# Optimization experiments

Hardware: AMD Instinct MI355X
Metric: run time of the kernel (lower is better)

The kernel has to match this reference:

```python
import jax, jax.numpy as jnp
import numpy as np

B, D, E, C = 16384, 2048, 16, 64  # batch, feat_dim, num_experts, classes per expert
CLASS_STARTS = np.arange(E, dtype=np.int32) * C  # contiguous equal-size class ranges


def setup_inputs() -> dict:
    key = jax.random.key(0)
    k1, k2, k3, k4, k5 = jax.random.split(key, 5)
    return {
        "features": jax.random.normal(k1, (B, D), dtype=jnp.float32),
        "coarse_w": jax.random.normal(k2, (E, D), dtype=jnp.float32) * 0.02,
        "coarse_b": jax.random.normal(k3, (E,), dtype=jnp.float32) * 0.02,
        "expert_w": jax.random.normal(k4, (E, C, D), dtype=jnp.float32) * 0.02,
        "expert_b": jax.random.normal(k5, (E, C), dtype=jnp.float32) * 0.02,
    }


def reference(features, coarse_w, coarse_b, expert_w, expert_b):
    # coarse router: Linear(feat_dim -> num_experts)
    coarse_output = features @ coarse_w.T + coarse_b          # [B, E]
    expert_id = jnp.argmax(coarse_output, axis=1)             # [B] top-1 routing

    # all-expert heads as one batched GEMM, then select routed expert per sample
    # (same math as gather-by-mask + per-expert Linear + scatter-back loop)
    y_all = jnp.einsum('bd,ecd->bec', features, expert_w) + expert_b  # [B, E, C]
    y = jnp.take_along_axis(y_all, expert_id[:, None, None], axis=1)[:, 0, :]  # [B, C]

    # local_preds: softmax probs of the routed expert (all experts have C = max classes)
    local_preds = jax.nn.softmax(y, axis=1)                   # [B, C]

    # global prediction = local argmax + expert's class-range start
    starts = jnp.asarray(CLASS_STARTS)
    global_preds = (jnp.argmax(y, axis=1) + starts[expert_id]).astype(jnp.float32)  # [B]

    return coarse_output, expert_id, local_preds, global_preds
```

## Files before the change

kernel.cpp:

```cpp
#include <hip/hip_runtime.h>
#include <cstdint>

static constexpr int B_ = 16384;
static constexpr int D_ = 2048;
static constexpr int E_ = 16;
static constexpr int C_ = 64;
static constexpr int KCH = 32;
static constexpr int TR_E = 64;
static constexpr int SK_E = 4;
static constexpr int TR_C = 128;
static constexpr int SK_C = 8;
static constexpr int MAXITEMS = (B_ / TR_E) + E_;

template <int RPT, int CPT, int NC, int TR, int SK, bool FLAT>
__global__ __launch_bounds__(256) void gemm_tile(
    const float* __restrict__ feat, const float* __restrict__ Wall,
    const int* __restrict__ rowList, const int* __restrict__ cnt,
    const int* __restrict__ sched, const int* __restrict__ nItems,
    float* __restrict__ part0,
    float* __restrict__ partRest)
{
  constexpr int FITER = TR / 32;
  constexpr int WSLOTS = NC * 8;
  constexpr int WITER = (WSLOTS + 255) / 256;
  constexpr int CG = NC / CPT;

  __shared__ float fT[KCH * TR];
  __shared__ float wT[KCH * NC];
  __shared__ int rIdx[TR];

  const int tid = threadIdx.x;
  int e, tile, kz;
  if (FLAT) {
    const int b = blockIdx.x;
    kz = b % SK;
    const int item = b / SK;
    if (item >= *nItems) return;
    const int s = sched[item];
    e = s & 255;
    tile = s >> 8;
  } else {
    e = 0;
    tile = blockIdx.x;
    kz = blockIdx.z;
  }
  const int count = cnt ? cnt[e] : B_;

  if (tid < TR) {
    const int slot = tile * TR + tid;
    rIdx[tid] = (slot < count) ? (rowList ? rowList[e * B_ + slot] : slot) : 0;
  }
  __syncthreads();

  unsigned grows[FITER];
  int dcf[FITER], sbf[FITER];
#pragma unroll
  for (int i = 0; i < FITER; ++i) {
    const int idx = i * 256 + tid;
    const int rl = idx >> 3;
    dcf[i] = idx & 7;
    grows[i] = (unsigned)rIdx[rl];
    sbf[i] = (((rl >> 3) ^ dcf[i]) << 3) + (rl & 7);
  }
  int wc[WITER], wdc[WITER], wsb[WITER];
  bool wact[WITER];
#pragma unroll
  for (int i = 0; i < WITER; ++i) {
    const int idx = i * 256 + tid;
    wact[i] = idx < WSLOTS;
    const int c = (idx < WSLOTS) ? (idx >> 3) : 0;
    wc[i] = c;
    wdc[i] = idx & 7;
    wsb[i] = (((c >> 3) ^ (wdc[i] & (NC / 8 - 1))) << 3) + (c & 7);
  }

  const int cg = tid % CG;
  const int rg = tid / CG;

  float acc[RPT][CPT];
#pragma unroll
  for (int r = 0; r < RPT; ++r)
#pragma unroll
    for (int c = 0; c < CPT; ++c) acc[r][c] = 0.f;

  const float* We = Wall + (size_t)e * NC * D_;
  constexpr int KRANGE = D_ / SK;
  constexpr int NCH = KRANGE / KCH;
  const int k0 = kz * KRANGE;

  float4 pf[FITER], pw[WITER];
#pragma unroll
  for (int i = 0; i < FITER; ++i)
    pf[i] = *(const float4*)(feat + (size_t)grows[i] * D_ + k0 + dcf[i] * 4);
#pragma unroll
  for (int i = 0; i < WITER; ++i)
    if (wact[i])
      pw[i] = *(const float4*)(We + (size_t)wc[i] * D_ + k0 + wdc[i] * 4);

  for (int ch = 0; ch < NCH; ++ch) {
#pragma unroll
    for (int i = 0; i < FITER; ++i) {
      float* p = &fT[(dcf[i] * 4) * TR + sbf[i]];
      p[0 * TR] = pf[i].x;
      p[1 * TR] = pf[i].y;
      p[2 * TR] = pf[i].z;
      p[3 * TR] = pf[i].w;
    }
#pragma unroll
    for (int i = 0; i < WITER; ++i)
      if (wact[i]) {
        float* p = &wT[(wdc[i] * 4) * NC + wsb[i]];
        p[0 * NC] = pw[i].x;
        p[1 * NC] = pw[i].y;
        p[2 * NC] = pw[i].z;
        p[3 * NC] = pw[i].w;
      }
    __syncthreads();
    if (ch + 1 < NCH) {
      const int kb = k0 + (ch + 1) * KCH;
#pragma unroll
      for (int i = 0; i < FITER; ++i)
        pf[i] = *(const float4*)(feat + (size_t)grows[i] * D_ + kb + dcf[i] * 4);
#pragma unroll
      for (int i = 0; i < WITER; ++i)
        if (wact[i])
          pw[i] = *(const float4*)(We + (size_t)wc[i] * D_ + kb + wdc[i] * 4);
    }
#pragma unroll
    for (int dd = 0; dd < KCH; ++dd) {
      const int s = dd >> 2;
      const int sw = s & (NC / 8 - 1);
      float a[RPT], bb[CPT];
#pragma unroll
      for (int r4 = 0; r4 < RPT / 4; ++r4) {
        const int col = rg * RPT + r4 * 4;
        const float4 v =
            *(const float4*)&fT[dd * TR + (((col >> 3) ^ s) << 3) + (col & 7)];
        a[r4 * 4 + 0] = v.x;
        a[r4 * 4 + 1] = v.y;
        a[r4 * 4 + 2] = v.z;
        a[r4 * 4 + 3] = v.w;
      }
      if constexpr (CPT >= 4) {
#pragma unroll
        for (int c4 = 0; c4 < CPT / 4; ++c4) {
          const int col = cg * CPT + c4 * 4;
          const float4 v =
              *(const float4*)&wT[dd * NC + (((col >> 3) ^ sw) << 3) + (col & 7)];
          bb[c4 * 4 + 0] = v.x;
          bb[c4 * 4 + 1] = v.y;
          bb[c4 * 4 + 2] = v.z;
          bb[c4 * 4 + 3] = v.w;
        }
      } else {
        const int col = cg * 2;
        const float2 v =
            *(const float2*)&wT[dd * NC + (((col >> 3) ^ sw) << 3) + (col & 7)];
        bb[0] = v.x;
        bb[1] = v.y;
      }
#pragma unroll
      for (int r = 0; r < RPT; ++r)
#pragma unroll
        for (int c = 0; c < CPT; ++c) acc[r][c] += a[r] * bb[c];
    }
    __syncthreads();
  }

  float* pk = kz ? (partRest + (size_t)(kz - 1) * B_ * NC) : part0;
#pragma unroll
  for (int r = 0; r < RPT; ++r) {
    const int lrow = rg * RPT + r;
    const int slot = tile * TR + lrow;
    if (slot < count) {
      const int grow = rIdx[lrow];
      float* dst = pk + (size_t)grow * NC + cg * CPT;
      if constexpr (CPT >= 4) {
#pragma unroll
        for (int c4 = 0; c4 < CPT / 4; ++c4)
          *(float4*)(dst + c4 * 4) =
              make_float4(acc[r][c4 * 4 + 0], acc[r][c4 * 4 + 1],
                          acc[r][c4 * 4 + 2], acc[r][c4 * 4 + 3]);
      } else {
        *(float2*)dst = make_float2(acc[r][0], acc[r][1]);
      }
    }
  }
}

__global__ __launch_bounds__(256) void coarse_finish(
    const float* __restrict__ cpart0, const float* __restrict__ cpartRest,
    const float* __restrict__ cb, float* __restrict__ out0,
    float* __restrict__ out1, int* __restrict__ eidArr, int* __restrict__ cnt,
    int* __restrict__ rowList) {
  __shared__ int lcnt[E_];
  __shared__ int lbase[E_];
  const int tid = threadIdx.x;
  if (tid < E_) lcnt[tid] = 0;
  __syncthreads();
  const int row = blockIdx.x * 256 + tid;

  float v[E_];
#pragma unroll
  for (int j = 0; j < E_; ++j) v[j] = cb[j];
#pragma unroll
  for (int kz = 0; kz < SK_C; ++kz) {
    const float* p = (kz == 0) ? (cpart0 + (size_t)row * E_)
                               : (cpartRest + ((size_t)(kz - 1) * B_ + row) * E_);
#pragma unroll
    for (int j4 = 0; j4 < E_ / 4; ++j4) {
      const float4 t = *(const float4*)(p + j4 * 4);
      v[j4 * 4 + 0] += t.x;
      v[j4 * 4 + 1] += t.y;
      v[j4 * 4 + 2] += t.z;
      v[j4 * 4 + 3] += t.w;
    }
  }
  int best = 0;
  float bv = v[0];
#pragma unroll
  for (int j = 1; j < E_; ++j)
    if (v[j] > bv) { bv = v[j]; best = j; }

  float* o0 = out0 + (size_t)row * E_;
#pragma unroll
  for (int j4 = 0; j4 < E_ / 4; ++j4)
    *(float4*)(o0 + j4 * 4) = make_float4(v[j4 * 4 + 0], v[j4 * 4 + 1],
                                          v[j4 * 4 + 2], v[j4 * 4 + 3]);
  out1[row] = (float)best;
  eidArr[row] = best;

  const int lpos = atomicAdd(&lcnt[best], 1);
  __syncthreads();
  if (tid < E_) lbase[tid] = atomicAdd(&cnt[tid], lcnt[tid]);
  __syncthreads();
  rowList[best * B_ + lbase[best] + lpos] = row;
}

__global__ void make_schedule(const int* __restrict__ cnt,
                              int* __restrict__ sched,
                              int* __restrict__ nItems) {
  __shared__ int tiles[E_];
  __shared__ int offs[E_];
  const int t = threadIdx.x;
  if (t < E_) tiles[t] = (cnt[t] + TR_E - 1) / TR_E;
  __syncthreads();
  if (t == 0) {
    int acc = 0;
    for (int e = 0; e < E_; ++e) {
      offs[e] = acc;
      acc += tiles[e];
    }
    *nItems = acc;
  }
  __syncthreads();
  if (t < E_) {
    const int o = offs[t], n = tiles[t];
    for (int k = 0; k < n; ++k) sched[o + k] = t | (k << 8);
  }
}

__global__ __launch_bounds__(256) void finish_rows(
    const float* __restrict__ ypart0, const float* __restrict__ ypartRest,
    const float* __restrict__ eb, const int* __restrict__ eidArr,
    float* __restrict__ out2, float* __restrict__ out3) {
  const int lane = threadIdx.x & 63;
  const int row = (blockIdx.x * 256 + threadIdx.x) >> 6;
  const int eid = eidArr[row];

  float v = eb[eid * C_ + lane];
  v += ypart0[(size_t)row * C_ + lane];
#pragma unroll
  for (int kz = 1; kz < SK_E; ++kz)
    v += ypartRest[((size_t)(kz - 1) * B_ + row) * C_ + lane];

  float m = v;
#pragma unroll
  for (int off = 32; off; off >>= 1) m = fmaxf(m, __shfl_xor(m, off, 64));
  const float p = __expf(v - m);
  float s = p;
#pragma unroll
  for (int off = 32; off; off >>= 1) s += __shfl_xor(s, off, 64);
  out2[(size_t)row * C_ + lane] = p / s;

  float av = v;
  int ai = lane;
#pragma unroll
  for (int off = 32; off; off >>= 1) {
    const float ov = __shfl_xor(av, off, 64);
    const int oi = __shfl_xor(ai, off, 64);
    if (ov > av || (ov == av && oi < ai)) { av = ov; ai = oi; }
  }
  if (lane == 0) out3[row] = (float)(ai + (eid << 6));
}

extern "C" void kernel_launch(void* const* d_in, const int* in_sizes, int n_in,
                              void* d_out, int out_size, void* d_ws,
                              size_t ws_size, hipStream_t stream) {
  const float* feat = (const float*)d_in[0];
  const float* cw = (const float*)d_in[1];
  const float* cb = (const float*)d_in[2];
  const float* ew = (const float*)d_in[3];
  const float* eb = (const float*)d_in[4];

  float* out0 = (float*)d_out;
  float* out1 = out0 + (size_t)B_ * E_;
  float* out2 = out1 + B_;
  float* out3 = out2 + (size_t)B_ * C_;

  char* ws = (char*)d_ws;
  float* cpartRest = (float*)ws;
  float* ypartRest = cpartRest + (size_t)(SK_C - 1) * B_ * E_;
  int* rowList = (int*)(ypartRest + (size_t)(SK_E - 1) * B_ * C_);
  int* cnt = rowList + (size_t)E_ * B_;
  int* eidArr = cnt + 64;
  int* sched = eidArr + B_;
  int* nItems = sched + 512;

  hipMemsetAsync(cnt, 0, E_ * sizeof(int), stream);

  gemm_tile<4, 2, E_, TR_C, SK_C, false>
      <<<dim3(B_ / TR_C, 1, SK_C), 256, 0, stream>>>(
          feat, cw, nullptr, nullptr, nullptr, nullptr, out0, cpartRest);
  coarse_finish<<<B_ / 256, 256, 0, stream>>>(out0, cpartRest, cb, out0, out1,
                                              eidArr, cnt, rowList);
  make_schedule<<<1, 64, 0, stream>>>(cnt, sched, nItems);
  gemm_tile<4, 4, C_, TR_E, SK_E, true>
      <<<MAXITEMS * SK_E, 256, 0, stream>>>(feat, ew, rowList, cnt, sched,
                                            nItems, out2, ypartRest);
  finish_rows<<<(B_ * 64) / 256, 256, 0, stream>>>(out2, ypartRest, eb, eidArr,
                                                   out2, out3);
}
```

Baseline: 298.9 us.

## Fuse coarse router GEMM, argmax, bucketing and scheduling into one kernel

Replaces the split-K coarse GEMM, coarse_finish and make_schedule kernels with a single coarse_fused kernel. In it, each wave computes 4 full rows with a register shuffle-transpose reduction, then does the argmax and row bucketing, and the last block (found via an atomic done counter) builds the expert schedule. This removes two launches and the partial-sum round trip through global memory. The expert GEMM is also changed to a K chunk of 64, which halves its sync/chunk count at the cost of more shared memory. The risks are lower parallelism in the coarse GEMM (1024 blocks, each re-reading the full coarse weights from cache) and the correctness burden of the last-block pattern.

```diff
diff --git a/kernel.cpp b/kernel.cpp
--- a/kernel.cpp
+++ b/kernel.cpp
@@ -5,50 +5,212 @@
 static constexpr int D_ = 2048;
 static constexpr int E_ = 16;
 static constexpr int C_ = 64;
-static constexpr int KCH = 32;
 static constexpr int TR_E = 64;
 static constexpr int SK_E = 4;
-static constexpr int TR_C = 128;
-static constexpr int SK_C = 8;
+static constexpr int KCH_E = 64;
 static constexpr int MAXITEMS = (B_ / TR_E) + E_;
 
-template <int RPT, int CPT, int NC, int TR, int SK, bool FLAT>
-__global__ __launch_bounds__(256) void gemm_tile(
+__global__ __launch_bounds__(256) void coarse_fused(
+    const float* __restrict__ feat, const float* __restrict__ cw,
+    const float* __restrict__ cb, float* __restrict__ out0,
+    float* __restrict__ out1, int* __restrict__ eidArr, int* __restrict__ cnt,
+    int* __restrict__ done, int* __restrict__ rowList,
+    int* __restrict__ sched, int* __restrict__ nItems) {
+  __shared__ int lcnt[E_];
+  __shared__ int lbase[E_];
+  __shared__ int rowE[16];
+  __shared__ int rowP[16];
+  __shared__ int lastFlag;
+
+  const int tid = threadIdx.x;
+  const int lane = tid & 63;
+  const int wv = tid >> 6;
+  if (tid < E_) lcnt[tid] = 0;
+  if (tid == 0) lastFlag = 0;
+  __syncthreads();
+
+  const int rowBase = blockIdx.x * 16 + wv * 4;
+  const int le = ((lane & 1) << 3) | ((lane & 2) << 1) | ((lane & 4) >> 1) |
+                 ((lane & 8) >> 3);
+  const float cbr = cb[le];
+
+  const float* rp[4];
+#pragma unroll
+  for (int r = 0; r < 4; ++r)
+    rp[r] = feat + (size_t)(rowBase + r) * D_ + lane * 4;
+
+  float acc[4][16];
+#pragma unroll
+  for (int r = 0; r < 4; ++r)
+#pragma unroll
+    for (int j = 0; j < 16; ++j) acc[r][j] = 0.f;
+
+  float4 pf[4];
+#pragma unroll
+  for (int r = 0; r < 4; ++r) pf[r] = *(const float4*)(rp[r]);
+
+  for (int c = 0; c < 8; ++c) {
+    float4 f[4];
+#pragma unroll
+    for (int r = 0; r < 4; ++r) f[r] = pf[r];
+    if (c < 7) {
+#pragma unroll
+      for (int r = 0; r < 4; ++r)
+        pf[r] = *(const float4*)(rp[r] + (c + 1) * 256);
+    }
+    const float* wb = cw + c * 256 + lane * 4;
+#pragma unroll
+    for (int e4 = 0; e4 < 4; ++e4) {
+      float4 w[4];
+#pragma unroll
+      for (int j = 0; j < 4; ++j)
+        w[j] = *(const float4*)(wb + (size_t)(e4 * 4 + j) * D_);
+#pragma unroll
+      for (int j = 0; j < 4; ++j)
+#pragma unroll
+        for (int r = 0; r < 4; ++r) {
+          acc[r][e4 * 4 + j] += f[r].x * w[j].x;
+          acc[r][e4 * 4 + j] += f[r].y * w[j].y;
+          acc[r][e4 * 4 + j] += f[r].z * w[j].z;
+          acc[r][e4 * 4 + j] += f[r].w * w[j].w;
+        }
+    }
+  }
+
+#pragma unroll
+  for (int r = 0; r < 4; ++r) {
+    float v[16];
+#pragma unroll
+    for (int j = 0; j < 16; ++j) v[j] = acc[r][j];
+    {
+      const bool hi = lane & 1;
+#pragma unroll
+      for (int j = 0; j < 8; ++j) {
+        const float a = v[j], b = v[j + 8];
+        v[j] = hi ? b : a;
+        v[j + 8] = hi ? a : b;
+      }
+#pragma unroll
+      for (int j = 0; j < 8; ++j) v[j] += __shfl_xor(v[j + 8], 1);
+    }
+    {
+      const bool hi = lane & 2;
+#pragma unroll
+      for (int j = 0; j < 4; ++j) {
+        const float a = v[j], b = v[j + 4];
+        v[j] = hi ? b : a;
+        v[j + 4] = hi ? a : b;
+      }
+#pragma unroll
+      for (int j = 0; j < 4; ++j) v[j] += __shfl_xor(v[j + 4], 2);
+    }
+    {
+      const bool hi = lane & 4;
+#pragma unroll
+      for (int j = 0; j < 2; ++j) {
+        const float a = v[j], b = v[j + 2];
+        v[j] = hi ? b : a;
+        v[j + 2] = hi ? a : b;
+      }
+#pragma unroll
+      for (int j = 0; j < 2; ++j) v[j] += __shfl_xor(v[j + 2], 4);
+    }
+    {
+      const bool hi = lane & 8;
+      const float a = v[0], b = v[1];
+      v[0] = hi ? b : a;
+      v[1] = hi ? a : b;
+      v[0] += __shfl_xor(v[1], 8);
+    }
+    v[0] += __shfl_xor(v[0], 16);
+    v[0] += __shfl_xor(v[0], 32);
+    const float val = v[0] + cbr;
+
+    const int row = rowBase + r;
+    if (lane < 16) out0[(size_t)row * E_ + le] = val;
+
+    float mv = val;
+    int mi = le;
+#pragma unroll
+    for (int d = 1; d <= 8; d <<= 1) {
+      const float ov = __shfl_xor(mv, d);
+      const int oi = __shfl_xor(mi, d);
+      if (ov > mv || (ov == mv && oi < mi)) {
+        mv = ov;
+        mi = oi;
+      }
+    }
+    if (lane == 0) {
+      out1[row] = (float)mi;
+      eidArr[row] = mi;
+      const int p = atomicAdd(&lcnt[mi], 1);
+      rowE[wv * 4 + r] = mi;
+      rowP[wv * 4 + r] = p;
+    }
+  }
+  __syncthreads();
+  if (tid < E_) lbase[tid] = atomicAdd(&cnt[tid], lcnt[tid]);
+  __syncthreads();
+  if (tid < 16) {
+    const int e = rowE[tid], p = rowP[tid];
+    rowList[e * B_ + lbase[e] + p] = blockIdx.x * 16 + tid;
+  }
+
+  __threadfence();
+  if (tid == 0) {
+    if (atomicAdd(done, 1) == (int)gridDim.x - 1) lastFlag = 1;
+  }
+  __syncthreads();
+  if (lastFlag) {
+    if (tid < E_) lcnt[tid] = (atomicAdd(&cnt[tid], 0) + TR_E - 1) / TR_E;
+    __syncthreads();
+    if (tid == 0) {
+      int a = 0;
+      for (int e = 0; e < E_; ++e) {
+        lbase[e] = a;
+        a += lcnt[e];
+      }
+      *nItems = a;
+    }
+    __syncthreads();
+    if (tid < E_) {
+      const int o = lbase[tid], n = lcnt[tid];
+      for (int k = 0; k < n; ++k) sched[o + k] = tid | (k << 8);
+    }
+  }
+}
+
+template <int RPT, int CPT, int NC, int TR, int SK, int KCH>
+__global__ __launch_bounds__(256) void gemm_expert(
     const float* __restrict__ feat, const float* __restrict__ Wall,
     const int* __restrict__ rowList, const int* __restrict__ cnt,
     const int* __restrict__ sched, const int* __restrict__ nItems,
-    float* __restrict__ part0,
-    float* __restrict__ partRest)
-{
-  constexpr int FITER = TR / 32;
-  constexpr int WSLOTS = NC * 8;
+    float* __restrict__ part0, float* __restrict__ partRest) {
+  constexpr int DCB = KCH / 4;
+  constexpr int FITER = TR * DCB / 256;
+  constexpr int WSLOTS = NC * DCB;
   constexpr int WITER = (WSLOTS + 255) / 256;
   constexpr int CG = NC / CPT;
+  constexpr int RB = TR / 8;
+  constexpr int CB = NC / 8;
 
   __shared__ float fT[KCH * TR];
   __shared__ float wT[KCH * NC];
   __shared__ int rIdx[TR];
 
   const int tid = threadIdx.x;
-  int e, tile, kz;
-  if (FLAT) {
-    const int b = blockIdx.x;
-    kz = b % SK;
-    const int item = b / SK;
-    if (item >= *nItems) return;
-    const int s = sched[item];
-    e = s & 255;
-    tile = s >> 8;
-  } else {
-    e = 0;
-    tile = blockIdx.x;
-    kz = blockIdx.z;
-  }
-  const int count = cnt ? cnt[e] : B_;
+  const int b = blockIdx.x;
+  const int kz = b % SK;
+  const int item = b / SK;
+  if (item >= *nItems) return;
+  const int s = sched[item];
+  const int e = s & 255;
+  const int tile = s >> 8;
+  const int count = cnt[e];
 
   if (tid < TR) {
     const int slot = tile * TR + tid;
-    rIdx[tid] = (slot < count) ? (rowList ? rowList[e * B_ + slot] : slot) : 0;
+    rIdx[tid] = (slot < count) ? rowList[e * B_ + slot] : 0;
   }
   __syncthreads();
 
@@ -57,21 +219,19 @@
 #pragma unroll
   for (int i = 0; i < FITER; ++i) {
     const int idx = i * 256 + tid;
-    const int rl = idx >> 3;
-    dcf[i] = idx & 7;
+    const int rl = idx / DCB;
+    dcf[i] = idx % DCB;
     grows[i] = (unsigned)rIdx[rl];
-    sbf[i] = (((rl >> 3) ^ dcf[i]) << 3) + (rl & 7);
+    sbf[i] = (((rl >> 3) ^ (dcf[i] & (RB - 1))) << 3) + (rl & 7);
   }
   int wc[WITER], wdc[WITER], wsb[WITER];
-  bool wact[WITER];
 #pragma unroll
   for (int i = 0; i < WITER; ++i) {
     const int idx = i * 256 + tid;
-    wact[i] = idx < WSLOTS;
-    const int c = (idx < WSLOTS) ? (idx >> 3) : 0;
+    const int c = idx / DCB;
     wc[i] = c;
-    wdc[i] = idx & 7;
-    wsb[i] = (((c >> 3) ^ (wdc[i] & (NC / 8 - 1))) << 3) + (c & 7);
+    wdc[i] = idx % DCB;
+    wsb[i] = (((c >> 3) ^ (wdc[i] & (CB - 1))) << 3) + (c & 7);
   }
 
   const int cg = tid % CG;
@@ -94,8 +254,7 @@
     pf[i] = *(const float4*)(feat + (size_t)grows[i] * D_ + k0 + dcf[i] * 4);
 #pragma unroll
   for (int i = 0; i < WITER; ++i)
-    if (wact[i])
-      pw[i] = *(const float4*)(We + (size_t)wc[i] * D_ + k0 + wdc[i] * 4);
+    pw[i] = *(const float4*)(We + (size_t)wc[i] * D_ + k0 + wdc[i] * 4);
 
   for (int ch = 0; ch < NCH; ++ch) {
 #pragma unroll
@@ -107,14 +266,13 @@
       p[3 * TR] = pf[i].w;
     }
 #pragma unroll
-    for (int i = 0; i < WITER; ++i)
-      if (wact[i]) {
-        float* p = &wT[(wdc[i] * 4) * NC + wsb[i]];
-        p[0 * NC] = pw[i].x;
-        p[1 * NC] = pw[i].y;
-        p[2 * NC] = pw[i].z;
-        p[3 * NC] = pw[i].w;
-      }
+    for (int i = 0; i < WITER; ++i) {
+      float* p = &wT[(wdc[i] * 4) * NC + wsb[i]];
+      p[0 * NC] = pw[i].x;
+      p[1 * NC] = pw[i].y;
+      p[2 * NC] = pw[i].z;
+      p[3 * NC] = pw[i].w;
+    }
     __syncthreads();
     if (ch + 1 < NCH) {
       const int kb = k0 + (ch + 1) * KCH;
@@ -123,41 +281,32 @@
         pf[i] = *(const float4*)(feat + (size_t)grows[i] * D_ + kb + dcf[i] * 4);
 #pragma unroll
       for (int i = 0; i < WITER; ++i)
-        if (wact[i])
-          pw[i] = *(const float4*)(We + (size_t)wc[i] * D_ + kb + wdc[i] * 4);
+        pw[i] = *(const float4*)(We + (size_t)wc[i] * D_ + kb + wdc[i] * 4);
     }
 #pragma unroll
     for (int dd = 0; dd < KCH; ++dd) {
-      const int s = dd >> 2;
-      const int sw = s & (NC / 8 - 1);
+      const int sz = (dd >> 2) & (RB - 1);
+      const int sw = (dd >> 2) & (CB - 1);
       float a[RPT], bb[CPT];
 #pragma unroll
       for (int r4 = 0; r4 < RPT / 4; ++r4) {
         const int col = rg * RPT + r4 * 4;
         const float4 v =
-            *(const float4*)&fT[dd * TR + (((col >> 3) ^ s) << 3) + (col & 7)];
+            *(const float4*)&fT[dd * TR + (((col >> 3) ^ sz) << 3) + (col & 7)];
         a[r4 * 4 + 0] = v.x;
         a[r4 * 4 + 1] = v.y;
         a[r4 * 4 + 2] = v.z;
         a[r4 * 4 + 3] = v.w;
       }
-      if constexpr (CPT >= 4) {
-#pragma unroll
-        for (int c4 = 0; c4 < CPT / 4; ++c4) {
-          const int col = cg * CPT + c4 * 4;
-          const float4 v =
-              *(const float4*)&wT[dd * NC + (((col >> 3) ^ sw) << 3) + (col & 7)];
-          bb[c4 * 4 + 0] = v.x;
-          bb[c4 * 4 + 1] = v.y;
-          bb[c4 * 4 + 2] = v.z;
-          bb[c4 * 4 + 3] = v.w;
-        }
-      } else {
-        const int col = cg * 2;
-        const float2 v =
-            *(const float2*)&wT[dd * NC + (((col >> 3) ^ sw) << 3) + (col & 7)];
-        bb[0] = v.x;
-        bb[1] = v.y;
+#pragma unroll
+      for (int c4 = 0; c4 < CPT / 4; ++c4) {
+        const int col = cg * CPT + c4 * 4;
+        const float4 v =
+            *(const float4*)&wT[dd * NC + (((col >> 3) ^ sw) << 3) + (col & 7)];
+        bb[c4 * 4 + 0] = v.x;
+        bb[c4 * 4 + 1] = v.y;
+        bb[c4 * 4 + 2] = v.z;
+        bb[c4 * 4 + 3] = v.w;
       }
 #pragma unroll
       for (int r = 0; r < RPT; ++r)
@@ -175,88 +324,12 @@
     if (slot < count) {
       const int grow = rIdx[lrow];
       float* dst = pk + (size_t)grow * NC + cg * CPT;
-      if constexpr (CPT >= 4) {
-#pragma unroll
-        for (int c4 = 0; c4 < CPT / 4; ++c4)
-          *(float4*)(dst + c4 * 4) =
-              make_float4(acc[r][c4 * 4 + 0], acc[r][c4 * 4 + 1],
-                          acc[r][c4 * 4 + 2], acc[r][c4 * 4 + 3]);
-      } else {
-        *(float2*)dst = make_float2(acc[r][0], acc[r][1]);
-      }
-    }
-  }
-}
-
-__global__ __launch_bounds__(256) void coarse_finish(
-    const float* __restrict__ cpart0, const float* __restrict__ cpartRest,
-    const float* __restrict__ cb, float* __restrict__ out0,
-    float* __restrict__ out1, int* __restrict__ eidArr, int* __restrict__ cnt,
-    int* __restrict__ rowList) {
-  __shared__ int lcnt[E_];
-  __shared__ int lbase[E_];
-  const int tid = threadIdx.x;
-  if (tid < E_) lcnt[tid] = 0;
-  __syncthreads();
-  const int row = blockIdx.x * 256 + tid;
-
-  float v[E_];
-#pragma unroll
-  for (int j = 0; j < E_; ++j) v[j] = cb[j];
-#pragma unroll
-  for (int kz = 0; kz < SK_C; ++kz) {
-    const float* p = (kz == 0) ? (cpart0 + (size_t)row * E_)
-                               : (cpartRest + ((size_t)(kz - 1) * B_ + row) * E_);
-#pragma unroll
-    for (int j4 = 0; j4 < E_ / 4; ++j4) {
-      const float4 t = *(const float4*)(p + j4 * 4);
-      v[j4 * 4 + 0] += t.x;
-      v[j4 * 4 + 1] += t.y;
-      v[j4 * 4 + 2] += t.z;
-      v[j4 * 4 + 3] += t.w;
-    }
-  }
-  int best = 0;
-  float bv = v[0];
-#pragma unroll
-  for (int j = 1; j < E_; ++j)
-    if (v[j] > bv) { bv = v[j]; best = j; }
-
-  float* o0 = out0 + (size_t)row * E_;
-#pragma unroll
-  for (int j4 = 0; j4 < E_ / 4; ++j4)
-    *(float4*)(o0 + j4 * 4) = make_float4(v[j4 * 4 + 0], v[j4 * 4 + 1],
-                                          v[j4 * 4 + 2], v[j4 * 4 + 3]);
-  out1[row] = (float)best;
-  eidArr[row] = best;
-
-  const int lpos = atomicAdd(&lcnt[best], 1);
-  __syncthreads();
-  if (tid < E_) lbase[tid] = atomicAdd(&cnt[tid], lcnt[tid]);
-  __syncthreads();
-  rowList[best * B_ + lbase[best] + lpos] = row;
-}
-
-__global__ void make_schedule(const int* __restrict__ cnt,
-                              int* __restrict__ sched,
-                              int* __restrict__ nItems) {
-  __shared__ int tiles[E_];
-  __shared__ int offs[E_];
-  const int t = threadIdx.x;
-  if (t < E_) tiles[t] = (cnt[t] + TR_E - 1) / TR_E;
-  __syncthreads();
-  if (t == 0) {
-    int acc = 0;
-    for (int e = 0; e < E_; ++e) {
-      offs[e] = acc;
-      acc += tiles[e];
-    }
-    *nItems = acc;
-  }
-  __syncthreads();
-  if (t < E_) {
-    const int o = offs[t], n = tiles[t];
-    for (int k = 0; k < n; ++k) sched[o + k] = t | (k << 8);
+#pragma unroll
+      for (int c4 = 0; c4 < CPT / 4; ++c4)
+        *(float4*)(dst + c4 * 4) =
+            make_float4(acc[r][c4 * 4 + 0], acc[r][c4 * 4 + 1],
+                        acc[r][c4 * 4 + 2], acc[r][c4 * 4 + 3]);
+    }
   }
 }
 
@@ -276,20 +349,23 @@
 
   float m = v;
 #pragma unroll
-  for (int off = 32; off; off >>= 1) m = fmaxf(m, __shfl_xor(m, off, 64));
+  for (int off = 32; off; off >>= 1) m = fmaxf(m, __shfl_xor(m, off));
   const float p = __expf(v - m);
   float s = p;
 #pragma unroll
-  for (int off = 32; off; off >>= 1) s += __shfl_xor(s, off, 64);
+  for (int off = 32; off; off >>= 1) s += __shfl_xor(s, off);
   out2[(size_t)row * C_ + lane] = p / s;
 
   float av = v;
   int ai = lane;
 #pragma unroll
   for (int off = 32; off; off >>= 1) {
-    const float ov = __shfl_xor(av, off, 64);
-    const int oi = __shfl_xor(ai, off, 64);
-    if (ov > av || (ov == av && oi < ai)) { av = ov; ai = oi; }
+    const float ov = __shfl_xor(av, off);
+    const int oi = __shfl_xor(ai, off);
+    if (ov > av || (ov == av && oi < ai)) {
+      av = ov;
+      ai = oi;
+    }
   }
   if (lane == 0) out3[row] = (float)(ai + (eid << 6));
 }
@@ -309,23 +385,19 @@
   float* out3 = out2 + (size_t)B_ * C_;
 
   char* ws = (char*)d_ws;
-  float* cpartRest = (float*)ws;
-  float* ypartRest = cpartRest + (size_t)(SK_C - 1) * B_ * E_;
+  float* ypartRest = (float*)ws;
   int* rowList = (int*)(ypartRest + (size_t)(SK_E - 1) * B_ * C_);
   int* cnt = rowList + (size_t)E_ * B_;
+  int* done = cnt + E_;
   int* eidArr = cnt + 64;
   int* sched = eidArr + B_;
   int* nItems = sched + 512;
 
-  hipMemsetAsync(cnt, 0, E_ * sizeof(int), stream);
-
-  gemm_tile<4, 2, E_, TR_C, SK_C, false>
-      <<<dim3(B_ / TR_C, 1, SK_C), 256, 0, stream>>>(
-          feat, cw, nullptr, nullptr, nullptr, nullptr, out0, cpartRest);
-  coarse_finish<<<B_ / 256, 256, 0, stream>>>(out0, cpartRest, cb, out0, out1,
-                                              eidArr, cnt, rowList);
-  make_schedule<<<1, 64, 0, stream>>>(cnt, sched, nItems);
-  gemm_tile<4, 4, C_, TR_E, SK_E, true>
+  hipMemsetAsync(cnt, 0, 256, stream);
+
+  coarse_fused<<<B_ / 16, 256, 0, stream>>>(feat, cw, cb, out0, out1, eidArr,
+                                            cnt, done, rowList, sched, nItems);
+  gemm_expert<4, 4, C_, TR_E, SK_E, KCH_E>
       <<<MAXITEMS * SK_E, 256, 0, stream>>>(feat, ew, rowList, cnt, sched,
                                             nItems, out2, ypartRest);
   finish_rows<<<(B_ * 64) / 256, 256, 0, stream>>>(out2, ypartRest, eb, eidArr,
```

Result: slower. 411.4 us (+37.6%).
